# Kernel optimization log

Measured on AMD Instinct MI355X. Metric: run time of the kernel, lower is better.

Reference implementation:

```python
import jax, jax.numpy as jnp
import numpy as np
from jax import lax

B = 2048      # batch
EMB = 128     # embedding_size
NF = 200      # num_filters
NR = 10000    # num_roles
NV = 50000    # num_values
ARITY = 5
EPS = 1e-5    # BatchNorm eps (torch default)


def setup_inputs() -> dict:
    key = jax.random.key(0)
    ks = jax.random.split(key, 12)
    bound = float(np.sqrt(1.0 / EMB))
    emb_roles = jax.random.uniform(ks[0], (NR, EMB), jnp.float32, -bound, bound).at[0].set(0.0)
    emb_values = jax.random.uniform(ks[1], (NV, EMB), jnp.float32, -bound, bound).at[0].set(0.0)
    D = NF * (EMB - 2)
    return {
        "x_batch": jax.random.randint(ks[2], (B, 2 * ARITY), 0, 10000),
        "arity": ARITY,
        "mode": 0,
        "emb_roles": emb_roles,
        "emb_values": emb_values,
        "conv1_w": jax.random.normal(ks[3], (NF, 1, 3, 3), jnp.float32) * 0.1,
        "conv1_b": jnp.zeros((NF,), jnp.float32),
        "bn1_gamma": jnp.ones((NF,), jnp.float32),
        "bn1_beta": jnp.zeros((NF,), jnp.float32),
        "conv2_w": jax.random.normal(ks[4], (NF, 1, 5, 3), jnp.float32) * 0.1,
        "conv2_b": jnp.zeros((NF,), jnp.float32),
        "bn2_gamma": jnp.ones((NF,), jnp.float32),
        "bn2_beta": jnp.zeros((NF,), jnp.float32),
        "fc_w": jax.random.normal(ks[5], (1, D), jnp.float32) * float(np.sqrt(2.0 / (D + 1))),
        "fc_b": jnp.zeros((1,), jnp.float32),
    }


def _conv(x, w, b):
    # x: [N,1,H,E], w: [F,1,kh,3] -> [N,F,1,E-2] (VALID conv; kh == H)
    y = lax.conv_general_dilated(x, w, (1, 1), 'VALID',
                                 dimension_numbers=('NCHW', 'OIHW', 'NCHW'))
    return y + b[None, :, None, None]


def reference(x_batch, arity, mode, emb_roles, emb_values,
              conv1_w, conv1_b, bn1_gamma, bn1_beta,
              conv2_w, conv2_b, bn2_gamma, bn2_beta, fc_w, fc_b):
    n = x_batch.shape[0]
    roles = x_batch[:, 0::2]
    vals = x_batch[:, 1::2]
    fr = emb_roles[roles[:, :2]]    # [B,2,E]
    fv = emb_values[vals[:, :2]]    # [B,2,E]
    # (head_value, role, tail_value) rows -> [B,3,E]
    hrt = jnp.stack([fv[:, 0], fr[:, 0], fv[:, 1]], axis=1)

    # primary triple branch: conv1 + BatchNorm (batch stats) + ReLU
    y1 = _conv(hrt[:, None], conv1_w, conv1_b)[:, :, 0, :]   # [B,F,E-2]
    m1 = y1.mean(axis=(0, 2), keepdims=True)
    v1 = y1.var(axis=(0, 2), keepdims=True)
    y1 = jax.nn.relu((y1 - m1) * jax.lax.rsqrt(v1 + EPS)
                     * bn1_gamma[None, :, None] + bn1_beta[None, :, None])
    feats = y1.reshape(n, -1)[:, None, :]                    # [B,1,D]

    if arity > 2:
        k = arity - 2
        kr = emb_roles[roles[:, 2:]]   # [B,K,E]
        kv = emb_values[vals[:, 2:]]   # [B,K,E]
        e = hrt.shape[-1]
        hrt_b = jnp.broadcast_to(hrt[:, None], (n, k, 3, e))
        x2 = jnp.concatenate([hrt_b, kr[:, :, None, :], kv[:, :, None, :]], axis=2)  # [B,K,5,E]
        y2 = _conv(x2.reshape(n * k, 1, 5, e), conv2_w, conv2_b)[:, :, 0, :]
        y2 = y2.reshape(n, k, y2.shape[1], y2.shape[2])      # [B,K,F,E-2]
        # original loop batch-norms each kv slot independently -> stats over (batch, width) per slot
        m2 = y2.mean(axis=(0, 3), keepdims=True)
        v2 = y2.var(axis=(0, 3), keepdims=True)
        y2 = jax.nn.relu((y2 - m2) * jax.lax.rsqrt(v2 + EPS)
                         * bn2_gamma[None, None, :, None] + bn2_beta[None, None, :, None])
        feats = jnp.concatenate([feats, y2.reshape(n, k, -1)], axis=1)  # [B,arity-1,D]

    min_val = feats.min(axis=1)                              # [B,D]
    return min_val @ fc_w.T + fc_b                           # [B,1]
```

## Files before the change

kernel.cpp:

```cpp
#include <hip/hip_runtime.h>

#define BB 2048
#define EMB 128
#define NF 200
#define W_OUT 126
#define EPS 1e-5f

#define AW_OFF 0
#define FCWQ_BYTE_OFF 51200
#define FCWQ_FLOATS (50 * 2 * 64 * 4)
#define WS_NEED (FCWQ_BYTE_OFF + FCWQ_FLOATS * 4)

#define SPBS 4
#define STATS_BLOCKS (BB / SPBS)
#define SPBM 2
#define MAIN_BLOCKS (BB / SPBM)

typedef _Float16 half8 __attribute__((ext_vector_type(8)));
typedef float f32x4v __attribute__((ext_vector_type(4)));

__device__ __forceinline__ const float* rowptr(const int* __restrict__ xr, int r,
                                               const float* __restrict__ er,
                                               const float* __restrict__ ev) {
  if (r == 0) return ev + (size_t)xr[1] * EMB;
  if (r == 1) return er + (size_t)xr[0] * EMB;
  if (r == 2) return ev + (size_t)xr[3] * EMB;
  const int k = (r - 3) >> 1;
  return ((r - 3) & 1) ? ev + (size_t)xr[5 + 2 * k] * EMB
                       : er + (size_t)xr[4 + 2 * k] * EMB;
}

__global__ __launch_bounds__(256, 2) void stats_mfma(
    const int* __restrict__ xb, const float* __restrict__ er,
    const float* __restrict__ ev, float* __restrict__ gout) {
  __shared__ _Float16 Bt[SPBS][40][136];
  __shared__ float Gred[SPBS][1024];
  const int tid = threadIdx.x;
  const int base = blockIdx.x * SPBS;

  for (int job = tid; job < SPBS * 136; job += 256) {
    const int s = job / 136, x = job % 136;
    if (x < W_OUT) {
      const int* xr = xb + (size_t)(base + s) * 10;
#pragma unroll
      for (int r = 0; r < 9; r++) {
        const float* hp = rowptr(xr, r, er, ev);
        Bt[s][3 * r + 0][x] = (_Float16)hp[x];
        Bt[s][3 * r + 1][x] = (_Float16)hp[x + 1];
        Bt[s][3 * r + 2][x] = (_Float16)hp[x + 2];
      }
      Bt[s][27][x] = (_Float16)1.0f;
#pragma unroll
      for (int k = 28; k < 40; k++) Bt[s][k][x] = (_Float16)0.f;
    } else {
#pragma unroll
      for (int k = 0; k < 40; k++) Bt[s][k][x] = (_Float16)0.f;
    }
  }
  __syncthreads();

  const int w = tid >> 6, l = tid & 63;
  const int tl = l & 15, kl = l >> 4;
  f32x4v a00 = {0.f, 0.f, 0.f, 0.f}, a01 = a00, a10 = a00, a11 = a00;
#pragma unroll
  for (int c = 0; c < 4; c++) {
    const int x0 = c * 32 + kl * 8;
    const half8 g0 = *(const half8*)&Bt[w][tl][x0];
    const half8 g1 = *(const half8*)&Bt[w][16 + tl][x0];
    a00 = __builtin_amdgcn_mfma_f32_16x16x32_f16(g0, g0, a00, 0, 0, 0);
    a01 = __builtin_amdgcn_mfma_f32_16x16x32_f16(g0, g1, a01, 0, 0, 0);
    a10 = __builtin_amdgcn_mfma_f32_16x16x32_f16(g1, g0, a10, 0, 0, 0);
    a11 = __builtin_amdgcn_mfma_f32_16x16x32_f16(g1, g1, a11, 0, 0, 0);
  }
#pragma unroll
  for (int r = 0; r < 4; r++) {
    const int rm = kl * 4 + r;
    Gred[w][rm * 32 + tl]             = a00[r];
    Gred[w][rm * 32 + 16 + tl]        = a01[r];
    Gred[w][(16 + rm) * 32 + tl]      = a10[r];
    Gred[w][(16 + rm) * 32 + 16 + tl] = a11[r];
  }
  __syncthreads();
  for (int idx = tid; idx < 1024; idx += 256) {
    float s = Gred[0][idx] + Gred[1][idx] + Gred[2][idx] + Gred[3][idx];
    atomicAdd(&gout[idx], s);
  }
}

__global__ __launch_bounds__(256) void swizzle_fcw(
    const float* __restrict__ fcw, float* __restrict__ fcwQ) {
  const int idx = blockIdx.x * 256 + threadIdx.x;
  if (idx >= FCWQ_FLOATS) return;
  const int mtile = idx >> 9;
  const int rem = idx & 511;
  const int jh = rem >> 8;
  const int rem2 = rem & 255;
  const int l = rem2 >> 2;
  const int j = rem2 & 3;
  const int f = mtile * 4 + (l >> 4);
  const int x = (jh * 4 + j) * 16 + (l & 15);
  fcwQ[idx] = (x < W_OUT) ? fcw[(size_t)f * W_OUT + x] : 0.f;
}

__global__ __launch_bounds__(256) void finalize_kernel(
    const float* __restrict__ w1, const float* __restrict__ w2,
    const float* __restrict__ g1, const float* __restrict__ be1,
    const float* __restrict__ g2, const float* __restrict__ be2,
    const float* __restrict__ gbuf, float* __restrict__ ws) {
  __shared__ float G[1024];
  const int tid = threadIdx.x;
  for (int e = tid; e < 1024; e += 256) G[e] = gbuf[e];
  __syncthreads();
  const int f = tid;
  if (f >= NF) return;
  _Float16* Aw = (_Float16*)ws + AW_OFF;
  float w1r[9], w2r[15];
#pragma unroll
  for (int j = 0; j < 9; j++)  w1r[j] = w1[f * 9 + j];
#pragma unroll
  for (int j = 0; j < 15; j++) w2r[j] = w2[f * 15 + j];
  const float invN = 1.0f / (float)(BB * W_OUT);

  float m1 = 0.f, q1 = 0.f;
#pragma unroll
  for (int i = 0; i < 9; i++) {
    m1 = fmaf(w1r[i], G[i * 32 + 27], m1);
#pragma unroll
    for (int j = 0; j < 9; j++) q1 = fmaf(w1r[i] * w1r[j], G[i * 32 + j], q1);
  }
  m1 *= invN;
  float v1 = q1 * invN - m1 * m1;
  float sc1 = g1[f] * rsqrtf(v1 + EPS);
  float sh1 = be1[f] - m1 * sc1;
  {
    _Float16* rw = Aw + (size_t)(4 * f + 0) * 32;
#pragma unroll
    for (int k = 0; k < 32; k++) rw[k] = (_Float16)0.f;
#pragma unroll
    for (int i = 0; i < 9; i++) rw[i] = (_Float16)(w1r[i] * sc1);
    rw[27] = (_Float16)sh1;
  }

  float mcm = 0.f, qc = 0.f;
#pragma unroll
  for (int i = 0; i < 9; i++) {
    mcm = fmaf(w2r[i], G[i * 32 + 27], mcm);
#pragma unroll
    for (int j = 0; j < 9; j++) qc = fmaf(w2r[i] * w2r[j], G[i * 32 + j], qc);
  }
#pragma unroll
  for (int kk = 0; kk < 3; kk++) {
    const int a = 3 + 2 * kk, b = 4 + 2 * kk;
    float m2 = mcm, cross = 0.f, qa = 0.f, qb = 0.f, qab = 0.f;
#pragma unroll
    for (int j = 0; j < 3; j++) {
      m2 = fmaf(w2r[9 + j],  G[(3 * a + j) * 32 + 27], m2);
      m2 = fmaf(w2r[12 + j], G[(3 * b + j) * 32 + 27], m2);
    }
#pragma unroll
    for (int i = 0; i < 9; i++) {
      float t = 0.f;
#pragma unroll
      for (int j = 0; j < 3; j++) {
        t = fmaf(w2r[9 + j],  G[i * 32 + 3 * a + j], t);
        t = fmaf(w2r[12 + j], G[i * 32 + 3 * b + j], t);
      }
      cross = fmaf(w2r[i], t, cross);
    }
#pragma unroll
    for (int j = 0; j < 3; j++)
#pragma unroll
      for (int jp = 0; jp < 3; jp++) {
        qa  = fmaf(w2r[9 + j]  * w2r[9 + jp],  G[(3 * a + j) * 32 + 3 * a + jp], qa);
        qb  = fmaf(w2r[12 + j] * w2r[12 + jp], G[(3 * b + j) * 32 + 3 * b + jp], qb);
        qab = fmaf(w2r[9 + j]  * w2r[12 + jp], G[(3 * a + j) * 32 + 3 * b + jp], qab);
      }
    float q2 = qc + 2.f * cross + qa + qb + 2.f * qab;
    float mean2 = m2 * invN;
    float v2 = q2 * invN - mean2 * mean2;
    float sck = g2[f] * rsqrtf(v2 + EPS);
    float shk = be2[f] - mean2 * sck;

    _Float16* rw = Aw + (size_t)(4 * f + 1 + kk) * 32;
#pragma unroll
    for (int k = 0; k < 32; k++) rw[k] = (_Float16)0.f;
#pragma unroll
    for (int i = 0; i < 9; i++) rw[i] = (_Float16)(w2r[i] * sck);
#pragma unroll
    for (int j = 0; j < 3; j++) {
      rw[3 * a + j] = (_Float16)(w2r[9 + j]  * sck);
      rw[3 * b + j] = (_Float16)(w2r[12 + j] * sck);
    }
    rw[27] = (_Float16)shk;
  }
}

template <bool SWZ>
__global__ __launch_bounds__(256, 4) void main_mfma(
    const int* __restrict__ xb, const float* __restrict__ er,
    const float* __restrict__ ev, const float* __restrict__ fcw,
    const float* __restrict__ fcwQ, const float* __restrict__ fcb,
    const float* __restrict__ ws, float* __restrict__ out) {
  __shared__ _Float16 Bm[SPBM][128][40];
  __shared__ float red[4];
  const int tid = threadIdx.x;
  const int base = blockIdx.x * SPBM;

  {
    const int s = tid >> 7, x = tid & 127;
    const int* xr = xb + (size_t)(base + s) * 10;
    const int x1 = (x + 1 < 128) ? x + 1 : 127;
    const int x2 = (x + 2 < 128) ? x + 2 : 127;
    _Float16* dst = &Bm[s][x][0];
#pragma unroll
    for (int r = 0; r < 9; r++) {
      const float* hp = rowptr(xr, r, er, ev);
      dst[3 * r + 0] = (_Float16)hp[x];
      dst[3 * r + 1] = (_Float16)hp[x1];
      dst[3 * r + 2] = (_Float16)hp[x2];
    }
    dst[27] = (_Float16)1.0f;
#pragma unroll
    for (int k = 28; k < 40; k++) dst[k] = (_Float16)0.f;
  }
  __syncthreads();

  const int w = tid >> 6, l = tid & 63;
  const int s = w >> 1, mh = w & 1;
  const int xl = l & 15, fl = l >> 4;
  const _Float16* __restrict__ Aw = (const _Float16*)ws + AW_OFF;
  const float4* __restrict__ fq4 = (const float4*)fcwQ;
  const float fcb0 = fcb[0];

  float psum = 0.f;
#pragma unroll 1
  for (int jh = 0; jh < 2; ++jh) {
    half8 bf[4];
#pragma unroll
    for (int j = 0; j < 4; ++j)
      bf[j] = *(const half8*)&Bm[s][(jh * 4 + j) * 16 + xl][fl * 8];
#pragma unroll 1
    for (int mtb = 0; mtb < 5; ++mtb) {
      half8 af[5];
#pragma unroll
      for (int i = 0; i < 5; ++i) {
        const int mtile = mh * 25 + mtb * 5 + i;
        af[i] = *(const half8*)&Aw[(size_t)(mtile * 16 + xl) * 32 + fl * 8];
      }
#pragma unroll
      for (int i = 0; i < 5; ++i) {
        const int mtile = mh * 25 + mtb * 5 + i;
        const int f = mtile * 4 + fl;
        float4 fq;
        if (SWZ) fq = fq4[(mtile * 2 + jh) * 64 + l];
#pragma unroll
        for (int j = 0; j < 4; ++j) {
          f32x4v acc = __builtin_amdgcn_mfma_f32_16x16x32_f16(
              af[i], bf[j], (f32x4v){0.f, 0.f, 0.f, 0.f}, 0, 0, 0);
          float fcv;
          if (SWZ) {
            fcv = (j == 0) ? fq.x : (j == 1) ? fq.y : (j == 2) ? fq.z : fq.w;
          } else {
            const int x = (jh * 4 + j) * 16 + xl;
            const bool xv = (x < W_OUT);
            const float fcl = fcw[(size_t)f * W_OUT + (xv ? x : 0)];
            fcv = xv ? fcl : 0.f;
          }
          float mv = fminf(fminf(acc[0], acc[1]), fminf(acc[2], acc[3]));
          psum = fmaf(fmaxf(mv, 0.f), fcv, psum);
        }
      }
    }
  }

#pragma unroll
  for (int off = 32; off; off >>= 1) psum += __shfl_xor(psum, off, 64);
  if (l == 0) red[w] = psum;
  __syncthreads();
  if (tid < SPBM)
    out[base + tid] = red[2 * tid] + red[2 * tid + 1] + fcb0;
}

extern "C" void kernel_launch(void* const* d_in, const int* in_sizes, int n_in,
                              void* d_out, int out_size, void* d_ws, size_t ws_size,
                              hipStream_t stream) {
  const int* xb    = (const int*)d_in[0];
  const float* er  = (const float*)d_in[3];
  const float* ev  = (const float*)d_in[4];
  const float* w1  = (const float*)d_in[5];
  const float* g1  = (const float*)d_in[7];
  const float* be1 = (const float*)d_in[8];
  const float* w2  = (const float*)d_in[9];
  const float* g2  = (const float*)d_in[11];
  const float* be2 = (const float*)d_in[12];
  const float* fcw = (const float*)d_in[13];
  const float* fcb = (const float*)d_in[14];
  float* ws  = (float*)d_ws;
  float* out = (float*)d_out;

  const int use_swz = (ws_size >= (size_t)WS_NEED) ? 1 : 0;
  float* fcwQ = (float*)((char*)d_ws + FCWQ_BYTE_OFF);

  hipMemsetAsync(out, 0, 1024 * sizeof(float), stream);
  if (use_swz)
    hipLaunchKernelGGL(swizzle_fcw, dim3((FCWQ_FLOATS + 255) / 256), dim3(256),
                       0, stream, fcw, fcwQ);
  hipLaunchKernelGGL(stats_mfma, dim3(STATS_BLOCKS), dim3(256), 0, stream,
                     xb, er, ev, out);
  hipLaunchKernelGGL(finalize_kernel, dim3(1), dim3(256), 0, stream,
                     w1, w2, g1, be1, g2, be2, out, ws);
  if (use_swz)
    hipLaunchKernelGGL((main_mfma<true>), dim3(MAIN_BLOCKS), dim3(256), 0,
                       stream, xb, er, ev, fcw, fcwQ, fcb, ws, out);
  else
    hipLaunchKernelGGL((main_mfma<false>), dim3(MAIN_BLOCKS), dim3(256), 0,
                       stream, xb, er, ev, fcw, fcwQ, fcb, ws, out);
}
```

Measured before the change: 57.37 us.

## Stage conv weights in LDS, store fc weights as fp16, nontemporal gathers

The main kernel now copies the 800x32 fp16 folded conv weight matrix from workspace into shared memory once per block, so A-fragment loads no longer go to global memory on every tile. The swizzled fc weights are stored as fp16 rather than fp32, which halves their read traffic. Embedding gathers use nontemporal loads, and launch bounds drop from 4 to 2 blocks per CU to fit the roughly 51 KB of added shared memory. The trade-offs are lower occupancy and an extra per-block global-to-LDS copy, plus some precision loss in the fc weights.

```diff
diff --git a/kernel.cpp b/kernel.cpp
--- a/kernel.cpp
+++ b/kernel.cpp
@@ -8,8 +8,8 @@
 
 #define AW_OFF 0
 #define FCWQ_BYTE_OFF 51200
-#define FCWQ_FLOATS (50 * 2 * 64 * 4)
-#define WS_NEED (FCWQ_BYTE_OFF + FCWQ_FLOATS * 4)
+#define FCWQ_HALFS (50 * 2 * 64 * 4)
+#define WS_NEED (FCWQ_BYTE_OFF + FCWQ_HALFS * 2)
 
 #define SPBS 4
 #define STATS_BLOCKS (BB / SPBS)
@@ -17,6 +17,7 @@
 #define MAIN_BLOCKS (BB / SPBM)
 
 typedef _Float16 half8 __attribute__((ext_vector_type(8)));
+typedef _Float16 half4v __attribute__((ext_vector_type(4)));
 typedef float f32x4v __attribute__((ext_vector_type(4)));
 
 __device__ __forceinline__ const float* rowptr(const int* __restrict__ xr, int r,
@@ -88,9 +89,9 @@
 }
 
 __global__ __launch_bounds__(256) void swizzle_fcw(
-    const float* __restrict__ fcw, float* __restrict__ fcwQ) {
+    const float* __restrict__ fcw, _Float16* __restrict__ fcwQh) {
   const int idx = blockIdx.x * 256 + threadIdx.x;
-  if (idx >= FCWQ_FLOATS) return;
+  if (idx >= FCWQ_HALFS) return;
   const int mtile = idx >> 9;
   const int rem = idx & 511;
   const int jh = rem >> 8;
@@ -99,7 +100,7 @@
   const int j = rem2 & 3;
   const int f = mtile * 4 + (l >> 4);
   const int x = (jh * 4 + j) * 16 + (l & 15);
-  fcwQ[idx] = (x < W_OUT) ? fcw[(size_t)f * W_OUT + x] : 0.f;
+  fcwQh[idx] = (_Float16)((x < W_OUT) ? fcw[(size_t)f * W_OUT + x] : 0.f);
 }
 
 __global__ __launch_bounds__(256) void finalize_kernel(
@@ -196,16 +197,23 @@
 }
 
 template <bool SWZ>
-__global__ __launch_bounds__(256, 4) void main_mfma(
+__global__ __launch_bounds__(256, 2) void main_mfma(
     const int* __restrict__ xb, const float* __restrict__ er,
     const float* __restrict__ ev, const float* __restrict__ fcw,
-    const float* __restrict__ fcwQ, const float* __restrict__ fcb,
+    const _Float16* __restrict__ fcwQh, const float* __restrict__ fcb,
     const float* __restrict__ ws, float* __restrict__ out) {
+  __shared__ _Float16 Af[800 * 32];
   __shared__ _Float16 Bm[SPBM][128][40];
   __shared__ float red[4];
   const int tid = threadIdx.x;
   const int base = blockIdx.x * SPBM;
 
+  {
+    const uint2* __restrict__ Ag = (const uint2*)ws;
+    uint2* Al = (uint2*)Af;
+#pragma unroll
+    for (int i = 0; i < 25; ++i) Al[tid + i * 256] = Ag[tid + i * 256];
+  }
   {
     const int s = tid >> 7, x = tid & 127;
     const int* xr = xb + (size_t)(base + s) * 10;
@@ -215,9 +223,12 @@
 #pragma unroll
     for (int r = 0; r < 9; r++) {
       const float* hp = rowptr(xr, r, er, ev);
-      dst[3 * r + 0] = (_Float16)hp[x];
-      dst[3 * r + 1] = (_Float16)hp[x1];
-      dst[3 * r + 2] = (_Float16)hp[x2];
+      const float v0 = __builtin_nontemporal_load(hp + x);
+      const float v1 = __builtin_nontemporal_load(hp + x1);
+      const float v2 = __builtin_nontemporal_load(hp + x2);
+      dst[3 * r + 0] = (_Float16)v0;
+      dst[3 * r + 1] = (_Float16)v1;
+      dst[3 * r + 2] = (_Float16)v2;
     }
     dst[27] = (_Float16)1.0f;
 #pragma unroll
@@ -228,8 +239,6 @@
   const int w = tid >> 6, l = tid & 63;
   const int s = w >> 1, mh = w & 1;
   const int xl = l & 15, fl = l >> 4;
-  const _Float16* __restrict__ Aw = (const _Float16*)ws + AW_OFF;
-  const float4* __restrict__ fq4 = (const float4*)fcwQ;
   const float fcb0 = fcb[0];
 
   float psum = 0.f;
@@ -245,21 +254,22 @@
 #pragma unroll
       for (int i = 0; i < 5; ++i) {
         const int mtile = mh * 25 + mtb * 5 + i;
-        af[i] = *(const half8*)&Aw[(size_t)(mtile * 16 + xl) * 32 + fl * 8];
+        af[i] = *(const half8*)&Af[(size_t)(mtile * 16 + xl) * 32 + fl * 8];
       }
 #pragma unroll
       for (int i = 0; i < 5; ++i) {
         const int mtile = mh * 25 + mtb * 5 + i;
         const int f = mtile * 4 + fl;
-        float4 fq;
-        if (SWZ) fq = fq4[(mtile * 2 + jh) * 64 + l];
+        half4v fqh;
+        if (SWZ)
+          fqh = *(const half4v*)&fcwQh[((size_t)(mtile * 2 + jh) * 64 + l) * 4];
 #pragma unroll
         for (int j = 0; j < 4; ++j) {
           f32x4v acc = __builtin_amdgcn_mfma_f32_16x16x32_f16(
               af[i], bf[j], (f32x4v){0.f, 0.f, 0.f, 0.f}, 0, 0, 0);
           float fcv;
           if (SWZ) {
-            fcv = (j == 0) ? fq.x : (j == 1) ? fq.y : (j == 2) ? fq.z : fq.w;
+            fcv = (float)fqh[j];
           } else {
             const int x = (jh * 4 + j) * 16 + xl;
             const bool xv = (x < W_OUT);
@@ -299,20 +309,20 @@
   float* out = (float*)d_out;
 
   const int use_swz = (ws_size >= (size_t)WS_NEED) ? 1 : 0;
-  float* fcwQ = (float*)((char*)d_ws + FCWQ_BYTE_OFF);
+  _Float16* fcwQh = (_Float16*)((char*)d_ws + FCWQ_BYTE_OFF);
 
   hipMemsetAsync(out, 0, 1024 * sizeof(float), stream);
   if (use_swz)
-    hipLaunchKernelGGL(swizzle_fcw, dim3((FCWQ_FLOATS + 255) / 256), dim3(256),
-                       0, stream, fcw, fcwQ);
+    hipLaunchKernelGGL(swizzle_fcw, dim3((FCWQ_HALFS + 255) / 256), dim3(256),
+                       0, stream, fcw, fcwQh);
   hipLaunchKernelGGL(stats_mfma, dim3(STATS_BLOCKS), dim3(256), 0, stream,
                      xb, er, ev, out);
   hipLaunchKernelGGL(finalize_kernel, dim3(1), dim3(256), 0, stream,
                      w1, w2, g1, be1, g2, be2, out, ws);
   if (use_swz)
     hipLaunchKernelGGL((main_mfma<true>), dim3(MAIN_BLOCKS), dim3(256), 0,
-                       stream, xb, er, ev, fcw, fcwQ, fcb, ws, out);
+                       stream, xb, er, ev, fcw, fcwQh, fcb, ws, out);
   else
     hipLaunchKernelGGL((main_mfma<false>), dim3(MAIN_BLOCKS), dim3(256), 0,
-                       stream, xb, er, ev, fcw, fcwQ, fcb, ws, out);
-}
+                       stream, xb, er, ev, fcw, fcwQh, fcb, ws, out);
+}
```

After: 57.14 us. Within noise of the previous version (-0.4%).
